# Performance work log

Measured on AMD Instinct MI355X. Metric: run time of the kernel, lower is better.

Reference implementation:

```python
import jax, jax.numpy as jnp
import numpy as np
import math

B, N, C = 32, 576, 1024
INNER, H = 256, 4
HD = INNER // H
ALPHA = 5.0
EPS = 1e-5

def _layer_norm(x, w, b):
    mu = jnp.mean(x, axis=-1, keepdims=True)
    var = jnp.mean((x - mu) ** 2, axis=-1, keepdims=True)
    return (x - mu) * jax.lax.rsqrt(var + EPS) * w + b

def setup_inputs() -> dict:
    key = jax.random.key(0)
    ks = jax.random.split(key, 20)
    def lin(k, out_d, in_d):
        scale = math.sqrt(6.0 / (in_d + out_d))
        return jax.random.uniform(k, (out_d, in_d), jnp.float32, -scale, scale)
    return {
        'query_features': jax.random.normal(ks[0], (B, N, C), jnp.float32),
        'support_features': jax.random.normal(ks[1], (B, N, C), jnp.float32),
        'support_mask_weights': jax.random.uniform(ks[2], (B, N), jnp.float32),
        'ln_q_w': jnp.ones((C,), jnp.float32), 'ln_q_b': jnp.zeros((C,), jnp.float32),
        'ln_s_w': jnp.ones((C,), jnp.float32), 'ln_s_b': jnp.zeros((C,), jnp.float32),
        'Wq': lin(ks[3], INNER, C), 'bq': jnp.zeros((INNER,), jnp.float32),
        'Wk': lin(ks[4], INNER, C), 'bk': jnp.zeros((INNER,), jnp.float32),
        'Wv': lin(ks[5], INNER, C), 'bv': jnp.zeros((INNER,), jnp.float32),
        'Wo': lin(ks[6], C, INNER), 'bo': jnp.zeros((C,), jnp.float32),
        'Wg': 0.02 * jax.random.normal(ks[7], (C, C), jnp.float32),
        'bg': jnp.full((C,), -1.0, jnp.float32),
    }

def reference(query_features, support_features, support_mask_weights,
              ln_q_w, ln_q_b, ln_s_w, ln_s_b,
              Wq, bq, Wk, bk, Wv, bv, Wo, bo, Wg, bg):
    q = _layer_norm(query_features, ln_q_w, ln_q_b)
    s = _layer_norm(support_features, ln_s_w, ln_s_b)
    Q = (q @ Wq.T + bq).reshape(B, N, H, HD).transpose(0, 2, 1, 3)  # (B,H,N,HD)
    K = (s @ Wk.T + bk).reshape(B, N, H, HD).transpose(0, 2, 1, 3)
    V = (s @ Wv.T + bv).reshape(B, N, H, HD).transpose(0, 2, 1, 3)
    logits = jnp.einsum('bhnd,bhmd->bhnm', Q, K) / math.sqrt(HD)
    logits = logits + ALPHA * support_mask_weights[:, None, None, :]
    attn = jax.nn.softmax(logits, axis=-1)
    ctx = jnp.einsum('bhnm,bhmd->bhnd', attn, V).transpose(0, 2, 1, 3).reshape(B, N, INNER)
    out = ctx @ Wo.T + bo
    gate = jax.nn.sigmoid(query_features @ Wg.T + bg)
    enhanced = query_features + gate * out
    return enhanced, attn
```

## Files before the change

kernel.cpp:

```cpp
#include <hip/hip_runtime.h>
#include <hip/hip_bf16.h>
#include <math.h>

#define B_ 32
#define N_ 576
#define C_ 1024
#define INNER_ 256
#define H_ 4
#define HD_ 64
#define M_ (B_*N_)
#define ALPHA_ 5.0f
#define EPS_ 1e-5f

typedef __attribute__((ext_vector_type(8))) short bf16x8;
typedef __attribute__((ext_vector_type(4))) float f32x4;
typedef __attribute__((ext_vector_type(4))) unsigned int u32x4;
typedef unsigned short u16;

__device__ inline u16 bfbits(float x) {
    union { __hip_bfloat16 h; u16 u; } c; c.h = __float2bfloat16(x); return c.u;
}
__device__ inline unsigned pack2bf(float a, float b) {
    return (unsigned)bfbits(a) | ((unsigned)bfbits(b) << 16);
}

__device__ __forceinline__ void gld16(void* lds, const void* g) {
    __builtin_amdgcn_global_load_lds(
        (const __attribute__((address_space(1))) unsigned int*)g,
        (__attribute__((address_space(3))) unsigned int*)lds, 16, 0, 0);
}

template<int GX, int GY>
__device__ inline void xcd_remap(int& col, int& row) {
    int f = blockIdx.y * GX + blockIdx.x;
    int xcd = f & 7;
    int slot = f >> 3;
    col = slot % GX;
    row = xcd * (GY >> 3) + slot / GX;
}

__global__ void ln_fused2_kernel(const float* __restrict__ Xq, const float* __restrict__ Xs,
                                 const float* __restrict__ wq, const float* __restrict__ bq,
                                 const float* __restrict__ ws, const float* __restrict__ bs,
                                 u16* __restrict__ outq, u16* __restrict__ outs,
                                 u16* __restrict__ outraw) {
    const float* X; const float* w; const float* b; u16* o;
    bool raw = (blockIdx.y == 0);
    if (raw) { X = Xq; w = wq; b = bq; o = outq; }
    else     { X = Xs; w = ws; b = bs; o = outs; }
    int row = blockIdx.x * 4 + (threadIdx.x >> 6);
    int lane = threadIdx.x & 63;
    const float* xp = X + (size_t)row * C_;
    float4 v[4];
    #pragma unroll
    for (int j = 0; j < 4; ++j) v[j] = *(const float4*)(xp + lane*4 + j*256);
    float s = 0.f, s2 = 0.f;
    #pragma unroll
    for (int j = 0; j < 4; ++j) {
        s  += v[j].x + v[j].y + v[j].z + v[j].w;
        s2 += v[j].x*v[j].x + v[j].y*v[j].y + v[j].z*v[j].z + v[j].w*v[j].w;
    }
    #pragma unroll
    for (int m = 32; m; m >>= 1) {
        s  += __shfl_xor(s,  m, 64);
        s2 += __shfl_xor(s2, m, 64);
    }
    float mean = s * (1.f/C_);
    float rs = rsqrtf(s2 * (1.f/C_) - mean*mean + EPS_);
    #pragma unroll
    for (int j = 0; j < 4; ++j) {
        int k = lane*4 + j*256;
        float4 wv = *(const float4*)(w + k);
        float4 bv = *(const float4*)(b + k);
        ushort4 ov;
        ov.x = bfbits((v[j].x - mean)*rs*wv.x + bv.x);
        ov.y = bfbits((v[j].y - mean)*rs*wv.y + bv.y);
        ov.z = bfbits((v[j].z - mean)*rs*wv.z + bv.z);
        ov.w = bfbits((v[j].w - mean)*rs*wv.w + bv.w);
        *(ushort4*)(o + (size_t)row*C_ + k) = ov;
        if (raw) {
            ushort4 r4;
            r4.x = bfbits(v[j].x); r4.y = bfbits(v[j].y);
            r4.z = bfbits(v[j].z); r4.w = bfbits(v[j].w);
            *(ushort4*)(outraw + (size_t)row*C_ + k) = r4;
        }
    }
}

__global__ void cvt_weights_kernel(const float* __restrict__ Wq, const float* __restrict__ Wk,
                                   const float* __restrict__ Wv, const float* __restrict__ Wo,
                                   const float* __restrict__ Wg,
                                   const float* __restrict__ bk, const float* __restrict__ bv,
                                   u16* __restrict__ Wq_b, u16* __restrict__ Wkv_b,
                                   u16* __restrict__ Wo_b, u16* __restrict__ Wg_b,
                                   float* __restrict__ bkv) {
    if (blockIdx.x == 0 && threadIdx.x < 128) {
        float4 t = (threadIdx.x < 64) ? ((const float4*)bk)[threadIdx.x]
                                      : ((const float4*)bv)[threadIdx.x - 64];
        ((float4*)bkv)[threadIdx.x] = t;
    }
    int g = blockIdx.x * 256 + threadIdx.x;
    const float* src; u16* dst; size_t off;
    if (g < 32768)       { src = Wq; dst = Wq_b;          off = (size_t)g*8; }
    else if (g < 65536)  { src = Wk; dst = Wkv_b;         off = (size_t)(g-32768)*8; }
    else if (g < 98304)  { src = Wv; dst = Wkv_b + 262144; off = (size_t)(g-65536)*8; }
    else if (g < 131072) { src = Wo; dst = Wo_b;          off = (size_t)(g-98304)*8; }
    else                 { src = Wg; dst = Wg_b;          off = (size_t)(g-131072)*8; }
    float4 a0 = *(const float4*)(src + off);
    float4 a1 = *(const float4*)(src + off + 4);
    union { u16 s[8]; u32x4 v; } o;
    o.s[0] = bfbits(a0.x); o.s[1] = bfbits(a0.y); o.s[2] = bfbits(a0.z); o.s[3] = bfbits(a0.w);
    o.s[4] = bfbits(a1.x); o.s[5] = bfbits(a1.y); o.s[6] = bfbits(a1.z); o.s[7] = bfbits(a1.w);
    *(u32x4*)(dst + off) = o.v;
}

template<int KDIM>
__device__ __forceinline__ void gemm_accum_async(const u16* __restrict__ A,
                                                 const u16* __restrict__ Bw,
                                                 int row0, int col0, int tid, int lane,
                                                 int wm, int wn,
                                                 u16 (&Asm)[128][64], u16 (&Bsm)[128][64],
                                                 f32x4 (&acc)[4][4]) {
    int rb = tid >> 3, cg = (tid & 7) * 8;
    for (int k0 = 0; k0 < KDIM; k0 += 64) {
        #pragma unroll
        for (int p = 0; p < 4; ++p) {
            int rr = p*32 + rb;
            gld16(&Asm[0][0] + ((size_t)(p*256 + tid))*8,
                  A + (size_t)(row0 + rr)*KDIM + k0 + cg);
            gld16(&Bsm[0][0] + ((size_t)(p*256 + tid))*8,
                  Bw + (size_t)(col0 + rr)*KDIM + k0 + cg);
        }
        __syncthreads();
        #pragma unroll
        for (int ks = 0; ks < 64; ks += 32) {
            bf16x8 af[4], bfr[4];
            #pragma unroll
            for (int i = 0; i < 4; ++i)
                af[i] = *(const bf16x8*)&Asm[wm + i*16 + (lane & 15)][ks + (lane >> 4)*8];
            #pragma unroll
            for (int j = 0; j < 4; ++j)
                bfr[j] = *(const bf16x8*)&Bsm[wn + j*16 + (lane & 15)][ks + (lane >> 4)*8];
            #pragma unroll
            for (int i = 0; i < 4; ++i)
                #pragma unroll
                for (int j = 0; j < 4; ++j)
                    acc[i][j] = __builtin_amdgcn_mfma_f32_16x16x32_bf16(
                        af[i], bfr[j], acc[i][j], 0, 0, 0);
        }
        __syncthreads();
    }
}

__global__ __launch_bounds__(256, 4)
void qkv_gemm_kernel(const u16* __restrict__ Aq, const u16* __restrict__ As,
                     const u16* __restrict__ Wq_b, const u16* __restrict__ Wkv_b,
                     const float* __restrict__ bq, const float* __restrict__ bkv,
                     u16* __restrict__ Qbf, u16* __restrict__ KVbf) {
    __shared__ u16 Asm[128][64];
    __shared__ u16 Bsm[128][64];
    int tid = threadIdx.x;
    int lane = tid & 63, wid = tid >> 6;
    int wm = (wid >> 1) * 64, wn = (wid & 1) * 64;
    int bc, br;
    xcd_remap<6, 144>(bc, br);
    int row0 = br * 128;
    bool isQ = (bc < 2);
    int col0 = (isQ ? bc : bc - 2) * 128;
    const u16* A  = isQ ? Aq   : As;
    const u16* Bw = isQ ? Wq_b : Wkv_b;
    const float* bias = isQ ? bq : bkv;
    u16* Out = isQ ? Qbf : KVbf;
    const int NOUT = isQ ? INNER_ : 2*INNER_;
    f32x4 acc[4][4] = {};
    gemm_accum_async<C_>(A, Bw, row0, col0, tid, lane, wm, wn, Asm, Bsm, acc);
    #pragma unroll
    for (int i = 0; i < 4; ++i) {
        #pragma unroll
        for (int j = 0; j < 4; ++j) {
            int col = col0 + wn + j*16 + (lane & 15);
            float bb = bias[col];
            #pragma unroll
            for (int r = 0; r < 4; ++r) {
                int row = row0 + wm + i*16 + (lane >> 4)*4 + r;
                Out[(size_t)row * NOUT + col] = bfbits(acc[i][j][r] + bb);
            }
        }
    }
}

__global__ __launch_bounds__(256, 3)
void final_fused_kernel(const float* __restrict__ query, const u16* __restrict__ Xq,
                        const u16* __restrict__ Wg_b, const float* __restrict__ bg,
                        const u16* __restrict__ ctxb, const u16* __restrict__ Wo_b,
                        const float* __restrict__ bo, float* __restrict__ out) {
    __shared__ u16 Asm[128][64];
    __shared__ u16 Bsm[128][64];
    int tid = threadIdx.x;
    int lane = tid & 63, wid = tid >> 6;
    int wm = (wid >> 1) * 64, wn = (wid & 1) * 64;
    int bc, br;
    xcd_remap<8, 144>(bc, br);
    int row0 = br * 128, col0 = bc * 128;
    f32x4 acc_o[4][4] = {};
    f32x4 acc_g[4][4] = {};
    gemm_accum_async<INNER_>(ctxb, Wo_b, row0, col0, tid, lane, wm, wn, Asm, Bsm, acc_o);
    gemm_accum_async<C_>(Xq, Wg_b, row0, col0, tid, lane, wm, wn, Asm, Bsm, acc_g);
    #pragma unroll
    for (int i = 0; i < 4; ++i) {
        #pragma unroll
        for (int j = 0; j < 4; ++j) {
            int col = col0 + wn + j*16 + (lane & 15);
            float bgv = bg[col], bov = bo[col];
            #pragma unroll
            for (int r = 0; r < 4; ++r) {
                int row = row0 + wm + i*16 + (lane >> 4)*4 + r;
                size_t idx = (size_t)row * C_ + col;
                float g = 1.f / (1.f + expf(-(acc_g[i][j][r] + bgv)));
                __builtin_nontemporal_store(query[idx] + g * (acc_o[i][j][r] + bov), &out[idx]);
            }
        }
    }
}

__device__ inline void stage_v_half(const u16* __restrict__ KV, u16* __restrict__ Vt,
                                    int b, int h, int HF, int tid) {
    #pragma unroll
    for (int i = 0; i < 9; ++i) {
        int c = tid + i*256;
        int k = c >> 3;
        int d0 = (c & 7) * 8;
        union { u32x4 v; u16 s[8]; } u;
        u.v = *(const u32x4*)(KV + ((size_t)(b*N_ + HF*288 + k))*512 + 256 + h*HD_ + d0);
        #pragma unroll
        for (int e = 0; e < 8; ++e)
            Vt[(d0 + e)*296 + k] = u.s[e];
    }
}

template<int HF>
__device__ inline void pv_half(const unsigned (&pk)[36][2], f32x4 (&cacc)[4],
                               const u16* __restrict__ Vt, int lane) {
    int s1 = (lane & 15) + ((lane & 16) << 1);
    int s2 = s1 + 16;
    bool hi = (lane & 32) != 0;
    #pragma unroll
    for (int t9 = 0; t9 < 9; ++t9) {
        const int t = HF*9 + t9;
        unsigned A01 = __shfl((int)pk[2*t  ][0], s1, 64);
        unsigned A23 = __shfl((int)pk[2*t  ][1], s1, 64);
        unsigned B01 = __shfl((int)pk[2*t+1][0], s1, 64);
        unsigned B23 = __shfl((int)pk[2*t+1][1], s1, 64);
        unsigned C01 = __shfl((int)pk[2*t  ][0], s2, 64);
        unsigned C23 = __shfl((int)pk[2*t  ][1], s2, 64);
        unsigned D01 = __shfl((int)pk[2*t+1][0], s2, 64);
        unsigned D23 = __shfl((int)pk[2*t+1][1], s2, 64);
        union { unsigned w[4]; bf16x8 v; } bu;
        bu.w[0] = hi ? B01 : A01;
        bu.w[1] = hi ? B23 : A23;
        bu.w[2] = hi ? D01 : C01;
        bu.w[3] = hi ? D23 : C23;
        int colb = 32*t - 288*HF + 8*(lane >> 4);
        #pragma unroll
        for (int dt = 0; dt < 4; ++dt) {
            bf16x8 a = *(const bf16x8*)&Vt[(16*dt + (lane & 15))*296 + colb];
            cacc[dt] = __builtin_amdgcn_mfma_f32_16x16x32_bf16(a, bu.v, cacc[dt], 0, 0, 0);
        }
    }
}

__global__ __launch_bounds__(256, 2)
void attn_mfma_kernel(const u16* __restrict__ Qbf, const u16* __restrict__ KV,
                      const float* __restrict__ mask,
                      float* __restrict__ attn_out, u16* __restrict__ ctxb) {
    __shared__ u16 Vt[64*296];
    __shared__ float Msk[576];
    int tid = threadIdx.x;
    int lane = tid & 63, wid = tid >> 6;
    int qb, bh;
    xcd_remap<9, 128>(qb, bh);
    int b = bh >> 2, h = bh & 3;
    int q0 = qb * 64;
    int g = lane >> 4;
    int qrow = q0 + wid*16 + (lane & 15);

    if (tid < 144) {
        float4 mv = *(const float4*)(mask + b*N_ + tid*4);
        *(float4*)&Msk[tid*4] = make_float4(ALPHA_*mv.x, ALPHA_*mv.y, ALPHA_*mv.z, ALPHA_*mv.w);
    }
    stage_v_half(KV, Vt, b, h, 0, tid);
    __syncthreads();

    const u16* qp = Qbf + ((size_t)(b*N_) + qrow)*INNER_ + h*HD_ + g*8;
    bf16x8 qf0 = *(const bf16x8*)qp;
    bf16x8 qf1 = *(const bf16x8*)(qp + 32);

    f32x4 acc[36];
    #pragma unroll
    for (int T = 0; T < 36; ++T) acc[T] = (f32x4){0.f, 0.f, 0.f, 0.f};

    const u16* kp = KV + ((size_t)(b*N_) + (lane & 15))*512 + h*HD_ + g*8;
    bf16x8 kb[2][2];
    kb[0][0] = *(const bf16x8*)(kp);
    kb[0][1] = *(const bf16x8*)(kp + 32);
    kb[1][0] = *(const bf16x8*)(kp + 16*512);
    kb[1][1] = *(const bf16x8*)(kp + 16*512 + 32);
    #pragma unroll
    for (int T = 0; T < 36; ++T) {
        bf16x8 n0, n1;
        if (T + 2 < 36) {
            n0 = *(const bf16x8*)(kp + (size_t)(T+2)*16*512);
            n1 = *(const bf16x8*)(kp + (size_t)(T+2)*16*512 + 32);
        }
        acc[T] = __builtin_amdgcn_mfma_f32_16x16x32_bf16(kb[T&1][0], qf0, acc[T], 0, 0, 0);
        acc[T] = __builtin_amdgcn_mfma_f32_16x16x32_bf16(kb[T&1][1], qf1, acc[T], 0, 0, 0);
        if (T + 2 < 36) { kb[T&1][0] = n0; kb[T&1][1] = n1; }
    }

    float m = -1e30f;
    #pragma unroll
    for (int T = 0; T < 36; ++T) {
        float4 mk = *(const float4*)&Msk[16*T + 4*g];
        acc[T][0] = acc[T][0]*0.125f + mk.x;
        acc[T][1] = acc[T][1]*0.125f + mk.y;
        acc[T][2] = acc[T][2]*0.125f + mk.z;
        acc[T][3] = acc[T][3]*0.125f + mk.w;
        m = fmaxf(m, fmaxf(fmaxf(acc[T][0], acc[T][1]), fmaxf(acc[T][2], acc[T][3])));
    }
    m = fmaxf(m, __shfl_xor(m, 16, 64));
    m = fmaxf(m, __shfl_xor(m, 32, 64));

    float l = 0.f;
    #pragma unroll
    for (int T = 0; T < 36; ++T) {
        acc[T][0] = expf(acc[T][0] - m);
        acc[T][1] = expf(acc[T][1] - m);
        acc[T][2] = expf(acc[T][2] - m);
        acc[T][3] = expf(acc[T][3] - m);
        l += acc[T][0] + acc[T][1] + acc[T][2] + acc[T][3];
    }
    l += __shfl_xor(l, 16, 64);
    l += __shfl_xor(l, 32, 64);
    float inv = 1.f / l;

    unsigned pk[36][2];
    float* ap = attn_out + ((size_t)bh*N_ + qrow)*N_;
    #pragma unroll
    for (int T = 0; T < 36; ++T) {
        float e0 = acc[T][0]*inv, e1 = acc[T][1]*inv;
        float e2 = acc[T][2]*inv, e3 = acc[T][3]*inv;
        f32x4 ov = {e0, e1, e2, e3};
        __builtin_nontemporal_store(ov, (f32x4*)(ap + 16*T + 4*g));
        pk[T][0] = pack2bf(e0, e1);
        pk[T][1] = pack2bf(e2, e3);
    }

    f32x4 cacc[4] = {};
    pv_half<0>(pk, cacc, Vt, lane);
    __syncthreads();
    stage_v_half(KV, Vt, b, h, 1, tid);
    __syncthreads();
    pv_half<1>(pk, cacc, Vt, lane);

    u16* cp = ctxb + ((size_t)(b*N_) + qrow)*INNER_ + h*HD_ + 4*g;
    #pragma unroll
    for (int dt = 0; dt < 4; ++dt) {
        ushort4 o;
        o.x = bfbits(cacc[dt][0]);
        o.y = bfbits(cacc[dt][1]);
        o.z = bfbits(cacc[dt][2]);
        o.w = bfbits(cacc[dt][3]);
        *(ushort4*)(cp + 16*dt) = o;
    }
}

extern "C" void kernel_launch(void* const* d_in, const int* in_sizes, int n_in,
                              void* d_out, int out_size, void* d_ws, size_t ws_size,
                              hipStream_t stream) {
    const float* query   = (const float*)d_in[0];
    const float* support = (const float*)d_in[1];
    const float* mask    = (const float*)d_in[2];
    const float* ln_q_w  = (const float*)d_in[3];
    const float* ln_q_b  = (const float*)d_in[4];
    const float* ln_s_w  = (const float*)d_in[5];
    const float* ln_s_b  = (const float*)d_in[6];
    const float* Wq      = (const float*)d_in[7];
    const float* bq      = (const float*)d_in[8];
    const float* Wk      = (const float*)d_in[9];
    const float* bk      = (const float*)d_in[10];
    const float* Wv      = (const float*)d_in[11];
    const float* bv      = (const float*)d_in[12];
    const float* Wo      = (const float*)d_in[13];
    const float* bo      = (const float*)d_in[14];
    const float* Wg      = (const float*)d_in[15];
    const float* bg      = (const float*)d_in[16];

    float* out      = (float*)d_out;
    float* attn_out = out + (size_t)M_ * C_;

    char* w = (char*)d_ws;
    u16* Aq    = (u16*)w;  w += (size_t)M_*C_*2;
    u16* As_   = (u16*)w;  w += (size_t)M_*C_*2;
    u16* Xq    = (u16*)w;  w += (size_t)M_*C_*2;
    u16* Wq_b  = (u16*)w;  w += (size_t)INNER_*C_*2;
    u16* Wkv_b = (u16*)w;  w += (size_t)2*INNER_*C_*2;
    u16* Wo_b  = (u16*)w;  w += (size_t)C_*INNER_*2;
    u16* Wg_b  = (u16*)w;  w += (size_t)C_*C_*2;
    float* bkv = (float*)w; w += 512*4;
    u16* Qbf   = (u16*)w;  w += (size_t)M_*INNER_*2;
    u16* KVbf  = (u16*)w;  w += (size_t)M_*2*INNER_*2;
    u16* ctxb  = (u16*)w;  w += (size_t)M_*INNER_*2;

    ln_fused2_kernel<<<dim3(M_/4, 2), dim3(256), 0, stream>>>(
        query, support, ln_q_w, ln_q_b, ln_s_w, ln_s_b, Aq, As_, Xq);

    cvt_weights_kernel<<<dim3(1024), dim3(256), 0, stream>>>(
        Wq, Wk, Wv, Wo, Wg, bk, bv, Wq_b, Wkv_b, Wo_b, Wg_b, bkv);

    qkv_gemm_kernel<<<dim3(6, 144), dim3(256), 0, stream>>>(
        Aq, As_, Wq_b, Wkv_b, bq, bkv, Qbf, KVbf);

    attn_mfma_kernel<<<dim3(N_/64, B_*H_), dim3(256), 0, stream>>>(
        Qbf, KVbf, mask, attn_out, ctxb);

    final_fused_kernel<<<dim3(8, 144), dim3(256), 0, stream>>>(
        query, Xq, Wg_b, bg, ctxb, Wo_b, bo, out);
}
```

Before: 324.2 us.

## Merge QKV and gate GEMMs into one kernel; slim final kernel to Wo GEMM

```diff
diff --git a/kernel.cpp b/kernel.cpp
--- a/kernel.cpp
+++ b/kernel.cpp
@@ -19,6 +19,9 @@
 
 __device__ inline u16 bfbits(float x) {
     union { __hip_bfloat16 h; u16 u; } c; c.h = __float2bfloat16(x); return c.u;
+}
+__device__ inline float bf2f(u16 u) {
+    union { unsigned u32; float f; } c; c.u32 = ((unsigned)u) << 16; return c.f;
 }
 __device__ inline unsigned pack2bf(float a, float b) {
     return (unsigned)bfbits(a) | ((unsigned)bfbits(b) << 16);
@@ -90,22 +93,14 @@
 __global__ void cvt_weights_kernel(const float* __restrict__ Wq, const float* __restrict__ Wk,
                                    const float* __restrict__ Wv, const float* __restrict__ Wo,
                                    const float* __restrict__ Wg,
-                                   const float* __restrict__ bk, const float* __restrict__ bv,
-                                   u16* __restrict__ Wq_b, u16* __restrict__ Wkv_b,
-                                   u16* __restrict__ Wo_b, u16* __restrict__ Wg_b,
-                                   float* __restrict__ bkv) {
-    if (blockIdx.x == 0 && threadIdx.x < 128) {
-        float4 t = (threadIdx.x < 64) ? ((const float4*)bk)[threadIdx.x]
-                                      : ((const float4*)bv)[threadIdx.x - 64];
-        ((float4*)bkv)[threadIdx.x] = t;
-    }
+                                   u16* __restrict__ Wall, u16* __restrict__ Wo_b) {
     int g = blockIdx.x * 256 + threadIdx.x;
     const float* src; u16* dst; size_t off;
-    if (g < 32768)       { src = Wq; dst = Wq_b;          off = (size_t)g*8; }
-    else if (g < 65536)  { src = Wk; dst = Wkv_b;         off = (size_t)(g-32768)*8; }
-    else if (g < 98304)  { src = Wv; dst = Wkv_b + 262144; off = (size_t)(g-65536)*8; }
+    if (g < 32768)       { src = Wq; dst = Wall;          off = (size_t)g*8; }
+    else if (g < 65536)  { src = Wk; dst = Wall + 262144; off = (size_t)(g-32768)*8; }
+    else if (g < 98304)  { src = Wv; dst = Wall + 524288; off = (size_t)(g-65536)*8; }
     else if (g < 131072) { src = Wo; dst = Wo_b;          off = (size_t)(g-98304)*8; }
-    else                 { src = Wg; dst = Wg_b;          off = (size_t)(g-131072)*8; }
+    else                 { src = Wg; dst = Wall + 786432; off = (size_t)(g-131072)*8; }
     float4 a0 = *(const float4*)(src + off);
     float4 a1 = *(const float4*)(src + off + 4);
     union { u16 s[8]; u32x4 v; } o;
@@ -114,110 +109,129 @@
     *(u32x4*)(dst + off) = o.v;
 }
 
-template<int KDIM>
-__device__ __forceinline__ void gemm_accum_async(const u16* __restrict__ A,
-                                                 const u16* __restrict__ Bw,
-                                                 int row0, int col0, int tid, int lane,
-                                                 int wm, int wn,
-                                                 u16 (&Asm)[128][64], u16 (&Bsm)[128][64],
-                                                 f32x4 (&acc)[4][4]) {
-    int rb = tid >> 3, cg = (tid & 7) * 8;
-    for (int k0 = 0; k0 < KDIM; k0 += 64) {
-        #pragma unroll
-        for (int p = 0; p < 4; ++p) {
-            int rr = p*32 + rb;
-            gld16(&Asm[0][0] + ((size_t)(p*256 + tid))*8,
-                  A + (size_t)(row0 + rr)*KDIM + k0 + cg);
-            gld16(&Bsm[0][0] + ((size_t)(p*256 + tid))*8,
-                  Bw + (size_t)(col0 + rr)*KDIM + k0 + cg);
-        }
-        __syncthreads();
-        #pragma unroll
-        for (int ks = 0; ks < 64; ks += 32) {
-            bf16x8 af[4], bfr[4];
-            #pragma unroll
-            for (int i = 0; i < 4; ++i)
-                af[i] = *(const bf16x8*)&Asm[wm + i*16 + (lane & 15)][ks + (lane >> 4)*8];
-            #pragma unroll
-            for (int j = 0; j < 4; ++j)
-                bfr[j] = *(const bf16x8*)&Bsm[wn + j*16 + (lane & 15)][ks + (lane >> 4)*8];
-            #pragma unroll
-            for (int i = 0; i < 4; ++i)
-                #pragma unroll
-                for (int j = 0; j < 4; ++j)
-                    acc[i][j] = __builtin_amdgcn_mfma_f32_16x16x32_bf16(
-                        af[i], bfr[j], acc[i][j], 0, 0, 0);
-        }
-        __syncthreads();
-    }
-}
-
-__global__ __launch_bounds__(256, 4)
-void qkv_gemm_kernel(const u16* __restrict__ Aq, const u16* __restrict__ As,
-                     const u16* __restrict__ Wq_b, const u16* __restrict__ Wkv_b,
-                     const float* __restrict__ bq, const float* __restrict__ bkv,
-                     u16* __restrict__ Qbf, u16* __restrict__ KVbf) {
-    __shared__ u16 Asm[128][64];
-    __shared__ u16 Bsm[128][64];
+__global__ __launch_bounds__(512, 4)
+void mega_gemm_kernel(const u16* __restrict__ Aq, const u16* __restrict__ As,
+                      const u16* __restrict__ Xq, const u16* __restrict__ Wall,
+                      const float* __restrict__ bq, const float* __restrict__ bk,
+                      const float* __restrict__ bv, const float* __restrict__ bg,
+                      u16* __restrict__ Qbf, u16* __restrict__ KVbf,
+                      u16* __restrict__ Gbf) {
+    __shared__ u16 Asm[256*32];
+    __shared__ u16 Bsm[128*32];
     int tid = threadIdx.x;
     int lane = tid & 63, wid = tid >> 6;
     int wm = (wid >> 1) * 64, wn = (wid & 1) * 64;
     int bc, br;
-    xcd_remap<6, 144>(bc, br);
-    int row0 = br * 128;
-    bool isQ = (bc < 2);
-    int col0 = (isQ ? bc : bc - 2) * 128;
-    const u16* A  = isQ ? Aq   : As;
-    const u16* Bw = isQ ? Wq_b : Wkv_b;
-    const float* bias = isQ ? bq : bkv;
-    u16* Out = isQ ? Qbf : KVbf;
-    const int NOUT = isQ ? INNER_ : 2*INNER_;
+    xcd_remap<14, 72>(bc, br);
+    int row0 = br * 256;
+    int wrow0 = bc * 128;
+    const u16* A = (bc < 2) ? Aq : (bc < 6) ? As : Xq;
+
     f32x4 acc[4][4] = {};
-    gemm_accum_async<C_>(A, Bw, row0, col0, tid, lane, wm, wn, Asm, Bsm, acc);
-    #pragma unroll
-    for (int i = 0; i < 4; ++i) {
-        #pragma unroll
-        for (int j = 0; j < 4; ++j) {
-            int col = col0 + wn + j*16 + (lane & 15);
-            float bb = bias[col];
+
+    int rA = tid >> 2;
+    int c8 = (tid & 3) * 8;
+
+    for (int k0 = 0; k0 < C_; k0 += 32) {
+        gld16(&Asm[(size_t)tid*8],         A + (size_t)(row0 + rA)*C_ + k0 + c8);
+        gld16(&Asm[(size_t)(512+tid)*8],   A + (size_t)(row0 + 128 + rA)*C_ + k0 + c8);
+        gld16(&Bsm[(size_t)tid*8],         Wall + (size_t)(wrow0 + rA)*C_ + k0 + c8);
+        __syncthreads();
+        bf16x8 af[4], bfv[4];
+        #pragma unroll
+        for (int i = 0; i < 4; ++i)
+            af[i] = *(const bf16x8*)&Asm[(wm + i*16 + (lane & 15))*32 + (lane >> 4)*8];
+        #pragma unroll
+        for (int j = 0; j < 4; ++j)
+            bfv[j] = *(const bf16x8*)&Bsm[(wn + j*16 + (lane & 15))*32 + (lane >> 4)*8];
+        #pragma unroll
+        for (int i = 0; i < 4; ++i)
+            #pragma unroll
+            for (int j = 0; j < 4; ++j)
+                acc[i][j] = __builtin_amdgcn_mfma_f32_16x16x32_bf16(
+                    af[i], bfv[j], acc[i][j], 0, 0, 0);
+        __syncthreads();
+    }
+
+    #pragma unroll
+    for (int j = 0; j < 4; ++j) {
+        int lc = wn + j*16 + (lane & 15);
+        int obc = wrow0 + lc;
+        float bb;
+        if (obc < 256)      bb = bq[obc];
+        else if (obc < 512) bb = bk[obc - 256];
+        else if (obc < 768) bb = bv[obc - 512];
+        else                bb = bg[obc - 768];
+        #pragma unroll
+        for (int i = 0; i < 4; ++i) {
             #pragma unroll
             for (int r = 0; r < 4; ++r) {
                 int row = row0 + wm + i*16 + (lane >> 4)*4 + r;
-                Out[(size_t)row * NOUT + col] = bfbits(acc[i][j][r] + bb);
+                float v = acc[i][j][r] + bb;
+                if (obc < 256)
+                    Qbf[(size_t)row*256 + obc] = bfbits(v);
+                else if (obc < 768)
+                    KVbf[(size_t)row*512 + (obc - 256)] = bfbits(v);
+                else
+                    Gbf[(size_t)row*1024 + (obc - 768)] =
+                        bfbits(1.f / (1.f + expf(-v)));
             }
         }
     }
 }
 
-__global__ __launch_bounds__(256, 3)
-void final_fused_kernel(const float* __restrict__ query, const u16* __restrict__ Xq,
-                        const u16* __restrict__ Wg_b, const float* __restrict__ bg,
-                        const u16* __restrict__ ctxb, const u16* __restrict__ Wo_b,
-                        const float* __restrict__ bo, float* __restrict__ out) {
-    __shared__ u16 Asm[128][64];
-    __shared__ u16 Bsm[128][64];
+__global__ __launch_bounds__(256, 2)
+void final_lite_kernel(const float* __restrict__ query, const u16* __restrict__ Gbf,
+                       const u16* __restrict__ ctxb, const u16* __restrict__ Wo_b,
+                       const float* __restrict__ bo, float* __restrict__ out) {
+    __shared__ u16 Asm[128][72];
+    __shared__ u16 Bsm[128][72];
     int tid = threadIdx.x;
     int lane = tid & 63, wid = tid >> 6;
     int wm = (wid >> 1) * 64, wn = (wid & 1) * 64;
     int bc, br;
     xcd_remap<8, 144>(bc, br);
     int row0 = br * 128, col0 = bc * 128;
-    f32x4 acc_o[4][4] = {};
-    f32x4 acc_g[4][4] = {};
-    gemm_accum_async<INNER_>(ctxb, Wo_b, row0, col0, tid, lane, wm, wn, Asm, Bsm, acc_o);
-    gemm_accum_async<C_>(Xq, Wg_b, row0, col0, tid, lane, wm, wn, Asm, Bsm, acc_g);
+    f32x4 acc[4][4] = {};
+    for (int k0 = 0; k0 < INNER_; k0 += 64) {
+        #pragma unroll
+        for (int i = 0; i < 4; ++i) {
+            int s = tid + i*256;
+            int r = s >> 3, cg = (s & 7) * 8;
+            *(u32x4*)&Asm[r][cg] = *(const u32x4*)(ctxb + (size_t)(row0 + r)*INNER_ + k0 + cg);
+            *(u32x4*)&Bsm[r][cg] = *(const u32x4*)(Wo_b + (size_t)(col0 + r)*INNER_ + k0 + cg);
+        }
+        __syncthreads();
+        #pragma unroll
+        for (int ks = 0; ks < 64; ks += 32) {
+            bf16x8 af[4], bfr[4];
+            #pragma unroll
+            for (int i = 0; i < 4; ++i)
+                af[i] = *(const bf16x8*)&Asm[wm + i*16 + (lane & 15)][ks + (lane >> 4)*8];
+            #pragma unroll
+            for (int j = 0; j < 4; ++j)
+                bfr[j] = *(const bf16x8*)&Bsm[wn + j*16 + (lane & 15)][ks + (lane >> 4)*8];
+            #pragma unroll
+            for (int i = 0; i < 4; ++i)
+                #pragma unroll
+                for (int j = 0; j < 4; ++j)
+                    acc[i][j] = __builtin_amdgcn_mfma_f32_16x16x32_bf16(
+                        af[i], bfr[j], acc[i][j], 0, 0, 0);
+        }
+        __syncthreads();
+    }
     #pragma unroll
     for (int i = 0; i < 4; ++i) {
         #pragma unroll
         for (int j = 0; j < 4; ++j) {
             int col = col0 + wn + j*16 + (lane & 15);
-            float bgv = bg[col], bov = bo[col];
+            float bov = bo[col];
             #pragma unroll
             for (int r = 0; r < 4; ++r) {
                 int row = row0 + wm + i*16 + (lane >> 4)*4 + r;
                 size_t idx = (size_t)row * C_ + col;
-                float g = 1.f / (1.f + expf(-(acc_g[i][j][r] + bgv)));
-                __builtin_nontemporal_store(query[idx] + g * (acc_o[i][j][r] + bov), &out[idx]);
+                float g = bf2f(Gbf[idx]);
+                __builtin_nontemporal_store(query[idx] + g * (acc[i][j][r] + bov), &out[idx]);
             }
         }
     }
@@ -402,27 +416,25 @@
     u16* Aq    = (u16*)w;  w += (size_t)M_*C_*2;
     u16* As_   = (u16*)w;  w += (size_t)M_*C_*2;
     u16* Xq    = (u16*)w;  w += (size_t)M_*C_*2;
-    u16* Wq_b  = (u16*)w;  w += (size_t)INNER_*C_*2;
-    u16* Wkv_b = (u16*)w;  w += (size_t)2*INNER_*C_*2;
+    u16* Wall  = (u16*)w;  w += (size_t)1792*C_*2;
     u16* Wo_b  = (u16*)w;  w += (size_t)C_*INNER_*2;
-    u16* Wg_b  = (u16*)w;  w += (size_t)C_*C_*2;
-    float* bkv = (float*)w; w += 512*4;
     u16* Qbf   = (u16*)w;  w += (size_t)M_*INNER_*2;
     u16* KVbf  = (u16*)w;  w += (size_t)M_*2*INNER_*2;
+    u16* Gbf   = (u16*)w;  w += (size_t)M_*C_*2;
     u16* ctxb  = (u16*)w;  w += (size_t)M_*INNER_*2;
 
     ln_fused2_kernel<<<dim3(M_/4, 2), dim3(256), 0, stream>>>(
         query, support, ln_q_w, ln_q_b, ln_s_w, ln_s_b, Aq, As_, Xq);
 
     cvt_weights_kernel<<<dim3(1024), dim3(256), 0, stream>>>(
-        Wq, Wk, Wv, Wo, Wg, bk, bv, Wq_b, Wkv_b, Wo_b, Wg_b, bkv);
-
-    qkv_gemm_kernel<<<dim3(6, 144), dim3(256), 0, stream>>>(
-        Aq, As_, Wq_b, Wkv_b, bq, bkv, Qbf, KVbf);
+        Wq, Wk, Wv, Wo, Wg, Wall, Wo_b);
+
+    mega_gemm_kernel<<<dim3(14, 72), dim3(512), 0, stream>>>(
+        Aq, As_, Xq, Wall, bq, bk, bv, bg, Qbf, KVbf, Gbf);
 
     attn_mfma_kernel<<<dim3(N_/64, B_*H_), dim3(256), 0, stream>>>(
         Qbf, KVbf, mask, attn_out, ctxb);
 
-    final_fused_kernel<<<dim3(8, 144), dim3(256), 0, stream>>>(
-        query, Xq, Wg_b, bg, ctxb, Wo_b, bo, out);
-}
+    final_lite_kernel<<<dim3(8, 144), dim3(256), 0, stream>>>(
+        query, Gbf, ctxb, Wo_b, bo, out);
+}
```

Measured after the change: 393.4 us. +21.3%, slower.
